# Performance work log

Measured on AMD Instinct MI355X. Metric: run time of the kernel, lower is better.

## Reference

```python
import jax, jax.numpy as jnp
import numpy as np

B, C, L = 8, 256, 2048
D = C // 8  # q/k channel dim = 32


def setup_inputs() -> dict:
    key = jax.random.key(0)
    kx, kq, kk, kv, kg = jax.random.split(key, 5)
    kq1, kq2 = jax.random.split(kq)
    kk1, kk2 = jax.random.split(kk)
    kv1, kv2 = jax.random.split(kv)
    s = 0.05
    return {
        "x": jax.random.normal(kx, (B, C, L), dtype=jnp.float32),
        "Wq": jax.random.normal(kq1, (D, C), dtype=jnp.float32) * s,
        "bq": jax.random.normal(kq2, (D,), dtype=jnp.float32) * s,
        "Wk": jax.random.normal(kk1, (D, C), dtype=jnp.float32) * s,
        "bk": jax.random.normal(kk2, (D,), dtype=jnp.float32) * s,
        "Wv": jax.random.normal(kv1, (C, C), dtype=jnp.float32) * s,
        "bv": jax.random.normal(kv2, (C,), dtype=jnp.float32) * s,
        "gamma": jax.random.normal(kg, (1,), dtype=jnp.float32) * 0.1,
    }


def reference(x, Wq, bq, Wk, bk, Wv, bv, gamma):
    # 1x1 Conv1d == per-position channel matmul
    Q = jnp.einsum("dc,bcl->bld", Wq, x) + bq            # (B, L, D)
    K = jnp.einsum("dc,bcl->bdl", Wk, x) + bk[:, None]   # (B, D, L)
    V = jnp.einsum("oc,bcl->bol", Wv, x) + bv[:, None]   # (B, C, L)
    scale = jnp.float32(1.0 / np.sqrt(D))
    # attn[b, i, j]: softmax over j (keys)
    attn = jax.nn.softmax(jnp.einsum("bid,bdj->bij", Q, K) * scale, axis=-1)
    # out = V @ attn^T : out[b, c, i] = sum_j V[b, c, j] * attn[b, i, j]
    out = jnp.einsum("bcj,bij->bci", V, attn)            # (B, C, L)
    return gamma * out + x
```

## Files before the change

### kernel.cpp

```cpp
#include <hip/hip_runtime.h>
#include <stdint.h>


#define BB 8
#define CC 256
#define LL 2048
#define DD 32

typedef unsigned short u16;
typedef __attribute__((ext_vector_type(8))) short short8;
typedef __attribute__((ext_vector_type(4))) float f32x4;

#define SCALE_LOG2E 0.2550348612f

static __device__ __forceinline__ uint32_t pack2bf16(float hi, float lo) {
    return (__float_as_uint(hi) & 0xFFFF0000u) | (__float_as_uint(lo) >> 16);
}

static __device__ __forceinline__ float fexp2(float v) {
#if __has_builtin(__builtin_amdgcn_exp2f)
    return __builtin_amdgcn_exp2f(v);
#else
    return exp2f(v);
#endif
}

static __device__ __forceinline__ float frcp(float v) {
#if __has_builtin(__builtin_amdgcn_rcpf)
    return __builtin_amdgcn_rcpf(v);
#else
    return 1.0f / v;
#endif
}

__global__ __launch_bounds__(256) void prep_w_kernel(
    const float* __restrict__ Wq, const float* __restrict__ Wk,
    const float* __restrict__ Wv, u16* __restrict__ Wh)
{
    int idx = blockIdx.x * 256 + threadIdx.x;
    int r = idx >> 6;
    int c4 = (idx & 63) << 2;
    const float* src;
    if (r < 32)       src = Wq + (size_t)r * CC + c4;
    else if (r < 64)  src = Wk + (size_t)(r - 32) * CC + c4;
    else              src = Wv + (size_t)(r - 64) * CC + c4;
    float4 v = *(const float4*)src;
    uint2 o;
    o.x = pack2bf16(v.y, v.x);
    o.y = pack2bf16(v.w, v.z);
    *(uint2*)(Wh + (size_t)r * CC + c4) = o;
}

__global__ __launch_bounds__(512, 2) void proj_kernel(
    const float* __restrict__ x, const u16* __restrict__ Wh,
    const float* __restrict__ bq, const float* __restrict__ bk,
    const float* __restrict__ bv,
    u16* __restrict__ Qh, u16* __restrict__ Kth, u16* __restrict__ Vh)
{
    __shared__ u16 xls[32 * 264];
    const int blk = blockIdx.x;
    const int b = blk & 7;
    const int l0 = (blk >> 3) << 5;
    const int tid = threadIdx.x;
    const int w = tid >> 6;
    const int lane = tid & 63;
    const int ln = lane & 15;
    const int q = lane >> 4;

#pragma unroll
    for (int cc = 0; cc < 4; ++cc) {
        const int c = cc * 64 + (tid >> 3);
        const int l4 = (tid & 7) * 4;
        const float4 v = *(const float4*)(x + ((size_t)(b * CC + c)) * LL + l0 + l4);
        xls[(l4 + 0) * 264 + c] = (u16)(__float_as_uint(v.x) >> 16);
        xls[(l4 + 1) * 264 + c] = (u16)(__float_as_uint(v.y) >> 16);
        xls[(l4 + 2) * 264 + c] = (u16)(__float_as_uint(v.z) >> 16);
        xls[(l4 + 3) * 264 + c] = (u16)(__float_as_uint(v.w) >> 16);
    }
    __syncthreads();

    const int wl = w & 1;
    const int wm = w >> 1;
    const int mbase = wm * 80;
    const int l = l0 + wl * 16 + ln;

    f32x4 acc[5];
#pragma unroll
    for (int i = 0; i < 5; ++i) acc[i] = (f32x4){0.f, 0.f, 0.f, 0.f};

#pragma unroll
    for (int c0 = 0; c0 < CC; c0 += 32) {
        const short8 bf = *(const short8*)(&xls[(wl * 16 + ln) * 264 + c0 + q * 8]);
#pragma unroll
        for (int mt = 0; mt < 5; ++mt) {
            const short8 af = *(const short8*)(Wh + (size_t)(mbase + mt * 16 + ln) * CC + c0 + q * 8);
            acc[mt] = __builtin_amdgcn_mfma_f32_16x16x32_bf16(af, bf, acc[mt], 0, 0, 0);
        }
    }

#pragma unroll
    for (int mt = 0; mt < 5; ++mt) {
        const int rg = mbase + mt * 16 + q * 4;
        if (rg < 32) {
            float v0 = (acc[mt][0] + bq[rg + 0]) * SCALE_LOG2E;
            float v1 = (acc[mt][1] + bq[rg + 1]) * SCALE_LOG2E;
            float v2 = (acc[mt][2] + bq[rg + 2]) * SCALE_LOG2E;
            float v3 = (acc[mt][3] + bq[rg + 3]) * SCALE_LOG2E;
            uint2 o; o.x = pack2bf16(v1, v0); o.y = pack2bf16(v3, v2);
            *(uint2*)(Qh + ((size_t)(b * LL) + l) * DD + rg) = o;
        } else if (rg < 64) {
            const int rk = rg - 32;
            float v0 = acc[mt][0] + bk[rk + 0];
            float v1 = acc[mt][1] + bk[rk + 1];
            float v2 = acc[mt][2] + bk[rk + 2];
            float v3 = acc[mt][3] + bk[rk + 3];
            uint2 o; o.x = pack2bf16(v1, v0); o.y = pack2bf16(v3, v2);
            *(uint2*)(Kth + ((size_t)(b * LL) + l) * DD + rk) = o;
        } else {
            const int cv = rg - 64;
#pragma unroll
            for (int rr = 0; rr < 4; ++rr) {
                const float v = acc[mt][rr] + bv[cv + rr];
                Vh[((size_t)(b * CC) + cv + rr) * LL + l] = (u16)(__float_as_uint(v) >> 16);
            }
        }
    }
}

__global__ __launch_bounds__(512, 1) void attn_kernel(
    const u16* __restrict__ Qh, const u16* __restrict__ Kth,
    const u16* __restrict__ Vh, const float* __restrict__ x,
    const float* __restrict__ gamma, float* __restrict__ out)
{
    __shared__ u16 pbuf[8 * 64 * 40];
    __shared__ float obuf[256 * 68];
    __shared__ float lbuf[8 * 64];

    const int blk = blockIdx.x;
    const int b = blk & 7;
    const int i0 = (blk >> 3) << 6;
    const int tid = threadIdx.x;
    const int w = tid >> 6;
    const int wc = w >> 2;
    const int wj = w & 3;
    const int lane = tid & 63;
    const int ln = lane & 15;
    const int q = lane >> 4;

    u16* pb = pbuf + w * (64 * 40);
    const u16* Qb = Qh + ((size_t)(b * LL) + i0) * DD;
    const u16* Kb = Kth + (size_t)(b * LL) * DD;
    const u16* Vb = Vh + ((size_t)(b * CC) + wc * 128) * LL;

    short8 qf[4];
#pragma unroll
    for (int it = 0; it < 4; ++it)
        qf[it] = *(const short8*)(Qb + (size_t)(it * 16 + ln) * DD + q * 8);

    const f32x4 zf = {0.f, 0.f, 0.f, 0.f};
    f32x4 oacc[8][4];
#pragma unroll
    for (int a = 0; a < 8; ++a)
#pragma unroll
        for (int c = 0; c < 4; ++c) oacc[a][c] = zf;
    float lsum[4] = {0.f, 0.f, 0.f, 0.f};

    int jb = wj * 32;
    short8 kf0 = *(const short8*)(Kb + (size_t)(jb + ln) * DD + q * 8);
    short8 kf1 = *(const short8*)(Kb + (size_t)(jb + 16 + ln) * DD + q * 8);

    for (int n = 0; n < 16; ++n) {
        jb = n * 128 + wj * 32;
        const int jnx = (n < 15) ? (n + 1) * 128 + wj * 32 : jb;

        short8 vf[8];
#pragma unroll
        for (int ct = 0; ct < 8; ++ct)
            vf[ct] = *(const short8*)(Vb + (size_t)(ct * 16 + ln) * LL + jb + q * 8);
        const short8 kn0 = *(const short8*)(Kb + (size_t)(jnx + ln) * DD + q * 8);
        const short8 kn1 = *(const short8*)(Kb + (size_t)(jnx + 16 + ln) * DD + q * 8);

#pragma unroll
        for (int jt = 0; jt < 2; ++jt) {
            const short8 kf = jt ? kf1 : kf0;
#pragma unroll
            for (int it = 0; it < 4; ++it) {
                const f32x4 st = __builtin_amdgcn_mfma_f32_16x16x32_bf16(kf, qf[it], zf, 0, 0, 0);
                const float e0 = fexp2(st[0]), e1 = fexp2(st[1]);
                const float e2 = fexp2(st[2]), e3 = fexp2(st[3]);
                lsum[it] += (e0 + e1) + (e2 + e3);
                uint2 d; d.x = pack2bf16(e1, e0); d.y = pack2bf16(e3, e2);
                *(uint2*)(&pb[(it * 16 + ln) * 40 + jt * 16 + q * 4]) = d;
            }
        }

        short8 pf[4];
#pragma unroll
        for (int it = 0; it < 4; ++it)
            pf[it] = *(const short8*)(&pb[(it * 16 + ln) * 40 + q * 8]);

#pragma unroll
        for (int ct = 0; ct < 8; ++ct)
#pragma unroll
            for (int it = 0; it < 4; ++it)
                oacc[ct][it] = __builtin_amdgcn_mfma_f32_16x16x32_bf16(vf[ct], pf[it], oacc[ct][it], 0, 0, 0);

        kf0 = kn0; kf1 = kn1;
    }

#pragma unroll
    for (int it = 0; it < 4; ++it) {
        float s = lsum[it];
        s += __shfl_xor(s, 16);
        s += __shfl_xor(s, 32);
        lsum[it] = s;
    }
    if (q == 0) {
#pragma unroll
        for (int it = 0; it < 4; ++it) lbuf[w * 64 + it * 16 + ln] = lsum[it];
    }

#pragma unroll
    for (int p = 0; p < 4; ++p) {
        if (wj == p) {
#pragma unroll
            for (int ct = 0; ct < 8; ++ct)
#pragma unroll
                for (int it = 0; it < 4; ++it) {
                    const int i = it * 16 + ln;
#pragma unroll
                    for (int r = 0; r < 4; ++r) {
                        const int c = wc * 128 + ct * 16 + q * 4 + r;
                        if (p == 0) obuf[c * 68 + i] = oacc[ct][it][r];
                        else        obuf[c * 68 + i] += oacc[ct][it][r];
                    }
                }
        }
        __syncthreads();
    }

    const float g = gamma[0];
    const int i4 = (tid & 15) * 4;
    float4 sv = {0.f, 0.f, 0.f, 0.f};
#pragma unroll
    for (int ww = 0; ww < 8; ++ww) {
        const float4 lv = *(const float4*)&lbuf[ww * 64 + i4];
        sv.x += lv.x; sv.y += lv.y; sv.z += lv.z; sv.w += lv.w;
    }
    float4 li;
    li.x = 2.0f * frcp(sv.x); li.y = 2.0f * frcp(sv.y);
    li.z = 2.0f * frcp(sv.z); li.w = 2.0f * frcp(sv.w);

#pragma unroll
    for (int cc = 0; cc < 8; ++cc) {
        const int c = cc * 32 + (tid >> 4);
        const float4 ov = *(const float4*)&obuf[c * 68 + i4];
        const size_t idx = ((size_t)(b * CC + c)) * LL + i0 + i4;
        const float4 xv = *(const float4*)(x + idx);
        float4 o;
        o.x = g * (ov.x * li.x) + xv.x;
        o.y = g * (ov.y * li.y) + xv.y;
        o.z = g * (ov.z * li.z) + xv.z;
        o.w = g * (ov.w * li.w) + xv.w;
        *(float4*)(out + idx) = o;
    }
}

extern "C" void kernel_launch(void* const* d_in, const int* in_sizes, int n_in,
                              void* d_out, int out_size, void* d_ws, size_t ws_size,
                              hipStream_t stream)
{
    const float* x     = (const float*)d_in[0];
    const float* Wq    = (const float*)d_in[1];
    const float* bq    = (const float*)d_in[2];
    const float* Wk    = (const float*)d_in[3];
    const float* bk    = (const float*)d_in[4];
    const float* Wv    = (const float*)d_in[5];
    const float* bv    = (const float*)d_in[6];
    const float* gamma = (const float*)d_in[7];
    float* out = (float*)d_out;

    uint8_t* ws = (uint8_t*)d_ws;
    u16* Wh  = (u16*)(ws + 0x000000);
    u16* Qh  = (u16*)(ws + 0x040000);
    u16* Kth = (u16*)(ws + 0x140000);
    u16* Vh  = (u16*)(ws + 0x240000);

    prep_w_kernel<<<80, 256, 0, stream>>>(Wq, Wk, Wv, Wh);
    proj_kernel<<<512, 512, 0, stream>>>(x, Wh, bq, bk, bv, Qh, Kth, Vh);
    attn_kernel<<<256, 512, 0, stream>>>(Qh, Kth, Vh, x, gamma, out);
}
```

Baseline: 149.4 us.

## Repartition attention across waves with shared P tile and no cross-wave reduction

The attention kernel now processes 32 queries per block over 512 blocks. Each of the 8 waves computes scores for a distinct 16-key slice and writes exp values into a double-buffered shared P tile. After a barrier, each wave multiplies its own 32 V channels against the full 128-key P tile. This removes the duplicated score/exp work across channel halves and the serialized four-phase shared-memory output reduction. In exchange it adds a block-wide barrier per key step, uses scalar output stores, and raises launch bounds to allow more resident blocks.

```diff
diff --git a/kernel.cpp b/kernel.cpp
--- a/kernel.cpp
+++ b/kernel.cpp
@@ -127,143 +127,116 @@
     }
 }
 
-__global__ __launch_bounds__(512, 1) void attn_kernel(
+#define PJ 136
+
+__global__ __launch_bounds__(512, 4) void attn_kernel(
     const u16* __restrict__ Qh, const u16* __restrict__ Kth,
     const u16* __restrict__ Vh, const float* __restrict__ x,
     const float* __restrict__ gamma, float* __restrict__ out)
 {
-    __shared__ u16 pbuf[8 * 64 * 40];
-    __shared__ float obuf[256 * 68];
-    __shared__ float lbuf[8 * 64];
+    __shared__ __attribute__((aligned(16))) u16 pbuf[2][32][PJ];
+    __shared__ float lbuf[8][32];
 
     const int blk = blockIdx.x;
     const int b = blk & 7;
-    const int i0 = (blk >> 3) << 6;
+    const int i0 = (blk >> 3) << 5;
     const int tid = threadIdx.x;
     const int w = tid >> 6;
-    const int wc = w >> 2;
-    const int wj = w & 3;
     const int lane = tid & 63;
     const int ln = lane & 15;
     const int q = lane >> 4;
 
-    u16* pb = pbuf + w * (64 * 40);
     const u16* Qb = Qh + ((size_t)(b * LL) + i0) * DD;
-    const u16* Kb = Kth + (size_t)(b * LL) * DD;
-    const u16* Vb = Vh + ((size_t)(b * CC) + wc * 128) * LL;
-
-    short8 qf[4];
-#pragma unroll
-    for (int it = 0; it < 4; ++it)
+    const u16* Kb = Kth + ((size_t)(b * LL) + w * 16 + ln) * DD + q * 8;
+    const u16* Vb = Vh + ((size_t)(b * CC) + w * 32) * LL;
+
+    short8 qf[2];
+#pragma unroll
+    for (int it = 0; it < 2; ++it)
         qf[it] = *(const short8*)(Qb + (size_t)(it * 16 + ln) * DD + q * 8);
 
     const f32x4 zf = {0.f, 0.f, 0.f, 0.f};
-    f32x4 oacc[8][4];
-#pragma unroll
-    for (int a = 0; a < 8; ++a)
-#pragma unroll
-        for (int c = 0; c < 4; ++c) oacc[a][c] = zf;
-    float lsum[4] = {0.f, 0.f, 0.f, 0.f};
-
-    int jb = wj * 32;
-    short8 kf0 = *(const short8*)(Kb + (size_t)(jb + ln) * DD + q * 8);
-    short8 kf1 = *(const short8*)(Kb + (size_t)(jb + 16 + ln) * DD + q * 8);
+    f32x4 oacc[2][2];
+#pragma unroll
+    for (int a = 0; a < 2; ++a)
+#pragma unroll
+        for (int c = 0; c < 2; ++c) oacc[a][c] = zf;
+    float lsum[2] = {0.f, 0.f};
+
+    short8 kf = *(const short8*)(Kb);
 
     for (int n = 0; n < 16; ++n) {
-        jb = n * 128 + wj * 32;
-        const int jnx = (n < 15) ? (n + 1) * 128 + wj * 32 : jb;
-
-        short8 vf[8];
-#pragma unroll
-        for (int ct = 0; ct < 8; ++ct)
-            vf[ct] = *(const short8*)(Vb + (size_t)(ct * 16 + ln) * LL + jb + q * 8);
-        const short8 kn0 = *(const short8*)(Kb + (size_t)(jnx + ln) * DD + q * 8);
-        const short8 kn1 = *(const short8*)(Kb + (size_t)(jnx + 16 + ln) * DD + q * 8);
-
-#pragma unroll
-        for (int jt = 0; jt < 2; ++jt) {
-            const short8 kf = jt ? kf1 : kf0;
-#pragma unroll
-            for (int it = 0; it < 4; ++it) {
-                const f32x4 st = __builtin_amdgcn_mfma_f32_16x16x32_bf16(kf, qf[it], zf, 0, 0, 0);
-                const float e0 = fexp2(st[0]), e1 = fexp2(st[1]);
-                const float e2 = fexp2(st[2]), e3 = fexp2(st[3]);
-                lsum[it] += (e0 + e1) + (e2 + e3);
-                uint2 d; d.x = pack2bf16(e1, e0); d.y = pack2bf16(e3, e2);
-                *(uint2*)(&pb[(it * 16 + ln) * 40 + jt * 16 + q * 4]) = d;
+        const int jb = n * 128;
+
+        short8 vf[2][4];
+#pragma unroll
+        for (int ct = 0; ct < 2; ++ct)
+#pragma unroll
+            for (int kk = 0; kk < 4; ++kk)
+                vf[ct][kk] = *(const short8*)(Vb + (size_t)(ct * 16 + ln) * LL + jb + kk * 32 + q * 8);
+        const short8 kn = *(const short8*)(Kb + (size_t)((n < 15 ? n + 1 : n) * 128) * DD);
+
+        u16* ps = &pbuf[n & 1][0][0];
+#pragma unroll
+        for (int it = 0; it < 2; ++it) {
+            const f32x4 st = __builtin_amdgcn_mfma_f32_16x16x32_bf16(kf, qf[it], zf, 0, 0, 0);
+            const float e0 = fexp2(st[0]), e1 = fexp2(st[1]);
+            const float e2 = fexp2(st[2]), e3 = fexp2(st[3]);
+            lsum[it] += (e0 + e1) + (e2 + e3);
+            uint2 d; d.x = pack2bf16(e1, e0); d.y = pack2bf16(e3, e2);
+            *(uint2*)(&ps[(it * 16 + ln) * PJ + w * 16 + q * 4]) = d;
+        }
+        __syncthreads();
+
+        __builtin_amdgcn_s_setprio(1);
+#pragma unroll
+        for (int kk = 0; kk < 4; ++kk) {
+            const short8 pf0 = *(const short8*)(&ps[(size_t)ln * PJ + kk * 32 + q * 8]);
+            const short8 pf1 = *(const short8*)(&ps[(size_t)(16 + ln) * PJ + kk * 32 + q * 8]);
+#pragma unroll
+            for (int ct = 0; ct < 2; ++ct) {
+                oacc[ct][0] = __builtin_amdgcn_mfma_f32_16x16x32_bf16(vf[ct][kk], pf0, oacc[ct][0], 0, 0, 0);
+                oacc[ct][1] = __builtin_amdgcn_mfma_f32_16x16x32_bf16(vf[ct][kk], pf1, oacc[ct][1], 0, 0, 0);
             }
         }
-
-        short8 pf[4];
-#pragma unroll
-        for (int it = 0; it < 4; ++it)
-            pf[it] = *(const short8*)(&pb[(it * 16 + ln) * 40 + q * 8]);
-
-#pragma unroll
-        for (int ct = 0; ct < 8; ++ct)
-#pragma unroll
-            for (int it = 0; it < 4; ++it)
-                oacc[ct][it] = __builtin_amdgcn_mfma_f32_16x16x32_bf16(vf[ct], pf[it], oacc[ct][it], 0, 0, 0);
-
-        kf0 = kn0; kf1 = kn1;
-    }
-
-#pragma unroll
-    for (int it = 0; it < 4; ++it) {
+        __builtin_amdgcn_s_setprio(0);
+        kf = kn;
+    }
+
+#pragma unroll
+    for (int it = 0; it < 2; ++it) {
         float s = lsum[it];
         s += __shfl_xor(s, 16);
         s += __shfl_xor(s, 32);
         lsum[it] = s;
     }
     if (q == 0) {
-#pragma unroll
-        for (int it = 0; it < 4; ++it) lbuf[w * 64 + it * 16 + ln] = lsum[it];
-    }
-
-#pragma unroll
-    for (int p = 0; p < 4; ++p) {
-        if (wj == p) {
-#pragma unroll
-            for (int ct = 0; ct < 8; ++ct)
-#pragma unroll
-                for (int it = 0; it < 4; ++it) {
-                    const int i = it * 16 + ln;
-#pragma unroll
-                    for (int r = 0; r < 4; ++r) {
-                        const int c = wc * 128 + ct * 16 + q * 4 + r;
-                        if (p == 0) obuf[c * 68 + i] = oacc[ct][it][r];
-                        else        obuf[c * 68 + i] += oacc[ct][it][r];
-                    }
-                }
-        }
-        __syncthreads();
+        lbuf[w][ln] = lsum[0];
+        lbuf[w][16 + ln] = lsum[1];
+    }
+    __syncthreads();
+
+    float linv[2];
+#pragma unroll
+    for (int it = 0; it < 2; ++it) {
+        float s = 0.f;
+#pragma unroll
+        for (int w8 = 0; w8 < 8; ++w8) s += lbuf[w8][it * 16 + ln];
+        linv[it] = frcp(s);
     }
 
     const float g = gamma[0];
-    const int i4 = (tid & 15) * 4;
-    float4 sv = {0.f, 0.f, 0.f, 0.f};
-#pragma unroll
-    for (int ww = 0; ww < 8; ++ww) {
-        const float4 lv = *(const float4*)&lbuf[ww * 64 + i4];
-        sv.x += lv.x; sv.y += lv.y; sv.z += lv.z; sv.w += lv.w;
-    }
-    float4 li;
-    li.x = 2.0f * frcp(sv.x); li.y = 2.0f * frcp(sv.y);
-    li.z = 2.0f * frcp(sv.z); li.w = 2.0f * frcp(sv.w);
-
-#pragma unroll
-    for (int cc = 0; cc < 8; ++cc) {
-        const int c = cc * 32 + (tid >> 4);
-        const float4 ov = *(const float4*)&obuf[c * 68 + i4];
-        const size_t idx = ((size_t)(b * CC + c)) * LL + i0 + i4;
-        const float4 xv = *(const float4*)(x + idx);
-        float4 o;
-        o.x = g * (ov.x * li.x) + xv.x;
-        o.y = g * (ov.y * li.y) + xv.y;
-        o.z = g * (ov.z * li.z) + xv.z;
-        o.w = g * (ov.w * li.w) + xv.w;
-        *(float4*)(out + idx) = o;
-    }
+#pragma unroll
+    for (int ct = 0; ct < 2; ++ct)
+#pragma unroll
+        for (int it = 0; it < 2; ++it) {
+#pragma unroll
+            for (int r = 0; r < 4; ++r) {
+                const int c = w * 32 + ct * 16 + q * 4 + r;
+                const size_t idx = ((size_t)(b * CC + c)) * LL + i0 + it * 16 + ln;
+                out[idx] = g * (oacc[ct][it][r] * linv[it]) + x[idx];
+            }
+        }
 }
 
 extern "C" void kernel_launch(void* const* d_in, const int* in_sizes, int n_in,
@@ -288,5 +261,5 @@
 
     prep_w_kernel<<<80, 256, 0, stream>>>(Wq, Wk, Wv, Wh);
     proj_kernel<<<512, 512, 0, stream>>>(x, Wh, bq, bk, bv, Qh, Kth, Vh);
-    attn_kernel<<<256, 512, 0, stream>>>(Qh, Kth, Vh, x, gamma, out);
-}
+    attn_kernel<<<512, 512, 0, stream>>>(Qh, Kth, Vh, x, gamma, out);
+}
```

After: 171.0 us. 1.14x slower.

## Halve attention query tile to 32 rows and raise occupancy with 512 blocks

Applied to the files above, without the earlier changes.

The attention kernel now processes 32 query rows per block instead of 64. This doubles the grid to 512 blocks and shrinks the accumulators, LDS buffers and register footprint, with launch bounds changed to allow 4 blocks per CU. The K software prefetch is dropped, and the V loads are split into two halves so the second half is issued after the score/exp phase. The intent is better latency hiding and CU fill through occupancy. In exchange, each block reuses K and V over half as many queries, doubling K/V reads across the grid.

```diff
diff --git a/kernel.cpp b/kernel.cpp
--- a/kernel.cpp
+++ b/kernel.cpp
@@ -127,18 +127,18 @@
     }
 }
 
-__global__ __launch_bounds__(512, 1) void attn_kernel(
+__global__ __launch_bounds__(512, 4) void attn_kernel(
     const u16* __restrict__ Qh, const u16* __restrict__ Kth,
     const u16* __restrict__ Vh, const float* __restrict__ x,
     const float* __restrict__ gamma, float* __restrict__ out)
 {
-    __shared__ u16 pbuf[8 * 64 * 40];
-    __shared__ float obuf[256 * 68];
-    __shared__ float lbuf[8 * 64];
+    __shared__ __attribute__((aligned(16))) u16 pbuf[8][32][40];
+    __shared__ float obuf[256][36];
+    __shared__ float lbuf[8][32];
 
     const int blk = blockIdx.x;
     const int b = blk & 7;
-    const int i0 = (blk >> 3) << 6;
+    const int i0 = (blk >> 3) << 5;
     const int tid = threadIdx.x;
     const int w = tid >> 6;
     const int wc = w >> 2;
@@ -147,44 +147,39 @@
     const int ln = lane & 15;
     const int q = lane >> 4;
 
-    u16* pb = pbuf + w * (64 * 40);
+    u16* pb = &pbuf[w][0][0];
     const u16* Qb = Qh + ((size_t)(b * LL) + i0) * DD;
     const u16* Kb = Kth + (size_t)(b * LL) * DD;
     const u16* Vb = Vh + ((size_t)(b * CC) + wc * 128) * LL;
 
-    short8 qf[4];
-#pragma unroll
-    for (int it = 0; it < 4; ++it)
+    short8 qf[2];
+#pragma unroll
+    for (int it = 0; it < 2; ++it)
         qf[it] = *(const short8*)(Qb + (size_t)(it * 16 + ln) * DD + q * 8);
 
     const f32x4 zf = {0.f, 0.f, 0.f, 0.f};
-    f32x4 oacc[8][4];
+    f32x4 oacc[8][2];
 #pragma unroll
     for (int a = 0; a < 8; ++a)
 #pragma unroll
-        for (int c = 0; c < 4; ++c) oacc[a][c] = zf;
-    float lsum[4] = {0.f, 0.f, 0.f, 0.f};
-
-    int jb = wj * 32;
-    short8 kf0 = *(const short8*)(Kb + (size_t)(jb + ln) * DD + q * 8);
-    short8 kf1 = *(const short8*)(Kb + (size_t)(jb + 16 + ln) * DD + q * 8);
+        for (int c = 0; c < 2; ++c) oacc[a][c] = zf;
+    float lsum[2] = {0.f, 0.f};
 
     for (int n = 0; n < 16; ++n) {
-        jb = n * 128 + wj * 32;
-        const int jnx = (n < 15) ? (n + 1) * 128 + wj * 32 : jb;
-
-        short8 vf[8];
-#pragma unroll
-        for (int ct = 0; ct < 8; ++ct)
-            vf[ct] = *(const short8*)(Vb + (size_t)(ct * 16 + ln) * LL + jb + q * 8);
-        const short8 kn0 = *(const short8*)(Kb + (size_t)(jnx + ln) * DD + q * 8);
-        const short8 kn1 = *(const short8*)(Kb + (size_t)(jnx + 16 + ln) * DD + q * 8);
+        const int jb = n * 128 + wj * 32;
+
+        short8 vf0[4];
+#pragma unroll
+        for (int ct = 0; ct < 4; ++ct)
+            vf0[ct] = *(const short8*)(Vb + (size_t)(ct * 16 + ln) * LL + jb + q * 8);
+        const short8 kf0 = *(const short8*)(Kb + (size_t)(jb + ln) * DD + q * 8);
+        const short8 kf1 = *(const short8*)(Kb + (size_t)(jb + 16 + ln) * DD + q * 8);
 
 #pragma unroll
         for (int jt = 0; jt < 2; ++jt) {
             const short8 kf = jt ? kf1 : kf0;
 #pragma unroll
-            for (int it = 0; it < 4; ++it) {
+            for (int it = 0; it < 2; ++it) {
                 const f32x4 st = __builtin_amdgcn_mfma_f32_16x16x32_bf16(kf, qf[it], zf, 0, 0, 0);
                 const float e0 = fexp2(st[0]), e1 = fexp2(st[1]);
                 const float e2 = fexp2(st[2]), e3 = fexp2(st[3]);
@@ -194,30 +189,38 @@
             }
         }
 
-        short8 pf[4];
-#pragma unroll
-        for (int it = 0; it < 4; ++it)
+        short8 vf1[4];
+#pragma unroll
+        for (int ct = 0; ct < 4; ++ct)
+            vf1[ct] = *(const short8*)(Vb + (size_t)((ct + 4) * 16 + ln) * LL + jb + q * 8);
+
+        short8 pf[2];
+#pragma unroll
+        for (int it = 0; it < 2; ++it)
             pf[it] = *(const short8*)(&pb[(it * 16 + ln) * 40 + q * 8]);
 
 #pragma unroll
-        for (int ct = 0; ct < 8; ++ct)
-#pragma unroll
-            for (int it = 0; it < 4; ++it)
-                oacc[ct][it] = __builtin_amdgcn_mfma_f32_16x16x32_bf16(vf[ct], pf[it], oacc[ct][it], 0, 0, 0);
-
-        kf0 = kn0; kf1 = kn1;
-    }
-
-#pragma unroll
-    for (int it = 0; it < 4; ++it) {
+        for (int ct = 0; ct < 4; ++ct)
+#pragma unroll
+            for (int it = 0; it < 2; ++it)
+                oacc[ct][it] = __builtin_amdgcn_mfma_f32_16x16x32_bf16(vf0[ct], pf[it], oacc[ct][it], 0, 0, 0);
+#pragma unroll
+        for (int ct = 0; ct < 4; ++ct)
+#pragma unroll
+            for (int it = 0; it < 2; ++it)
+                oacc[4 + ct][it] = __builtin_amdgcn_mfma_f32_16x16x32_bf16(vf1[ct], pf[it], oacc[4 + ct][it], 0, 0, 0);
+    }
+
+#pragma unroll
+    for (int it = 0; it < 2; ++it) {
         float s = lsum[it];
         s += __shfl_xor(s, 16);
         s += __shfl_xor(s, 32);
         lsum[it] = s;
     }
     if (q == 0) {
-#pragma unroll
-        for (int it = 0; it < 4; ++it) lbuf[w * 64 + it * 16 + ln] = lsum[it];
+        lbuf[w][ln] = lsum[0];
+        lbuf[w][16 + ln] = lsum[1];
     }
 
 #pragma unroll
@@ -226,13 +229,13 @@
 #pragma unroll
             for (int ct = 0; ct < 8; ++ct)
 #pragma unroll
-                for (int it = 0; it < 4; ++it) {
+                for (int it = 0; it < 2; ++it) {
                     const int i = it * 16 + ln;
 #pragma unroll
                     for (int r = 0; r < 4; ++r) {
                         const int c = wc * 128 + ct * 16 + q * 4 + r;
-                        if (p == 0) obuf[c * 68 + i] = oacc[ct][it][r];
-                        else        obuf[c * 68 + i] += oacc[ct][it][r];
+                        if (p == 0) obuf[c][i] = oacc[ct][it][r];
+                        else        obuf[c][i] += oacc[ct][it][r];
                     }
                 }
         }
@@ -240,11 +243,11 @@
     }
 
     const float g = gamma[0];
-    const int i4 = (tid & 15) * 4;
+    const int i4 = (tid & 7) * 4;
     float4 sv = {0.f, 0.f, 0.f, 0.f};
 #pragma unroll
     for (int ww = 0; ww < 8; ++ww) {
-        const float4 lv = *(const float4*)&lbuf[ww * 64 + i4];
+        const float4 lv = *(const float4*)&lbuf[ww][i4];
         sv.x += lv.x; sv.y += lv.y; sv.z += lv.z; sv.w += lv.w;
     }
     float4 li;
@@ -252,9 +255,9 @@
     li.z = 2.0f * frcp(sv.z); li.w = 2.0f * frcp(sv.w);
 
 #pragma unroll
-    for (int cc = 0; cc < 8; ++cc) {
-        const int c = cc * 32 + (tid >> 4);
-        const float4 ov = *(const float4*)&obuf[c * 68 + i4];
+    for (int cc = 0; cc < 4; ++cc) {
+        const int c = cc * 64 + (tid >> 3);
+        const float4 ov = *(const float4*)&obuf[c][i4];
         const size_t idx = ((size_t)(b * CC + c)) * LL + i0 + i4;
         const float4 xv = *(const float4*)(x + idx);
         float4 o;
@@ -288,5 +291,5 @@
 
     prep_w_kernel<<<80, 256, 0, stream>>>(Wq, Wk, Wv, Wh);
     proj_kernel<<<512, 512, 0, stream>>>(x, Wh, bq, bk, bv, Qh, Kth, Vh);
-    attn_kernel<<<256, 512, 0, stream>>>(Qh, Kth, Vh, x, gamma, out);
-}
+    attn_kernel<<<512, 512, 0, stream>>>(Qh, Kth, Vh, x, gamma, out);
+}
```

After: 174.8 us. 1.17x slower.

## Software-pipeline score and PV phases with double-buffered P; coalesce V stores

Applied to the files above, without the earlier changes.

The attention loop now computes the exp-scores for the next key block into a second LDS P buffer while the PV MFMAs for the current block run. This lets exp/VALU work interleave with matrix work, and K is prefetched two blocks ahead. The projection kernel stages V through LDS and writes it with 16-byte coalesced rows instead of scattered 2-byte stores. The cost is more LDS per block (a doubled pbuf plus a vls buffer) and some extra register pressure.

```diff
diff --git a/kernel.cpp b/kernel.cpp
--- a/kernel.cpp
+++ b/kernel.cpp
@@ -58,6 +58,7 @@
     u16* __restrict__ Qh, u16* __restrict__ Kth, u16* __restrict__ Vh)
 {
     __shared__ u16 xls[32 * 264];
+    __shared__ __attribute__((aligned(16))) u16 vls[256 * 40];
     const int blk = blockIdx.x;
     const int b = blk & 7;
     const int l0 = (blk >> 3) << 5;
@@ -83,6 +84,7 @@
     const int wm = w >> 1;
     const int mbase = wm * 80;
     const int l = l0 + wl * 16 + ln;
+    const int li = wl * 16 + ln;
 
     f32x4 acc[5];
 #pragma unroll
@@ -121,9 +123,21 @@
 #pragma unroll
             for (int rr = 0; rr < 4; ++rr) {
                 const float v = acc[mt][rr] + bv[cv + rr];
-                Vh[((size_t)(b * CC) + cv + rr) * LL + l] = (u16)(__float_as_uint(v) >> 16);
+                vls[(cv + rr) * 40 + li] = (u16)(__float_as_uint(v) >> 16);
             }
         }
+    }
+
+    __syncthreads();
+    {
+        const int row = tid >> 1;
+        const int h = (tid & 1) * 16;
+        const u16* src = &vls[row * 40 + h];
+        const uint4 v0 = *(const uint4*)(src);
+        const uint4 v1 = *(const uint4*)(src + 8);
+        uint4* dst = (uint4*)(Vh + ((size_t)(b * CC) + row) * LL + l0 + h);
+        dst[0] = v0;
+        dst[1] = v1;
     }
 }
 
@@ -132,7 +146,7 @@
     const u16* __restrict__ Vh, const float* __restrict__ x,
     const float* __restrict__ gamma, float* __restrict__ out)
 {
-    __shared__ u16 pbuf[8 * 64 * 40];
+    __shared__ __attribute__((aligned(16))) u16 pbuf[2][8][64 * 40];
     __shared__ float obuf[256 * 68];
     __shared__ float lbuf[8 * 64];
 
@@ -147,7 +161,6 @@
     const int ln = lane & 15;
     const int q = lane >> 4;
 
-    u16* pb = pbuf + w * (64 * 40);
     const u16* Qb = Qh + ((size_t)(b * LL) + i0) * DD;
     const u16* Kb = Kth + (size_t)(b * LL) * DD;
     const u16* Vb = Vh + ((size_t)(b * CC) + wc * 128) * LL;
@@ -165,24 +178,11 @@
         for (int c = 0; c < 4; ++c) oacc[a][c] = zf;
     float lsum[4] = {0.f, 0.f, 0.f, 0.f};
 
-    int jb = wj * 32;
-    short8 kf0 = *(const short8*)(Kb + (size_t)(jb + ln) * DD + q * 8);
-    short8 kf1 = *(const short8*)(Kb + (size_t)(jb + 16 + ln) * DD + q * 8);
-
-    for (int n = 0; n < 16; ++n) {
-        jb = n * 128 + wj * 32;
-        const int jnx = (n < 15) ? (n + 1) * 128 + wj * 32 : jb;
-
-        short8 vf[8];
-#pragma unroll
-        for (int ct = 0; ct < 8; ++ct)
-            vf[ct] = *(const short8*)(Vb + (size_t)(ct * 16 + ln) * LL + jb + q * 8);
-        const short8 kn0 = *(const short8*)(Kb + (size_t)(jnx + ln) * DD + q * 8);
-        const short8 kn1 = *(const short8*)(Kb + (size_t)(jnx + 16 + ln) * DD + q * 8);
-
+    auto Sphase = [&](int slot, short8 ka, short8 kb) {
+        u16* pw = &pbuf[slot][w][0];
 #pragma unroll
         for (int jt = 0; jt < 2; ++jt) {
-            const short8 kf = jt ? kf1 : kf0;
+            const short8 kf = jt ? kb : ka;
 #pragma unroll
             for (int it = 0; it < 4; ++it) {
                 const f32x4 st = __builtin_amdgcn_mfma_f32_16x16x32_bf16(kf, qf[it], zf, 0, 0, 0);
@@ -190,14 +190,37 @@
                 const float e2 = fexp2(st[2]), e3 = fexp2(st[3]);
                 lsum[it] += (e0 + e1) + (e2 + e3);
                 uint2 d; d.x = pack2bf16(e1, e0); d.y = pack2bf16(e3, e2);
-                *(uint2*)(&pb[(it * 16 + ln) * 40 + jt * 16 + q * 4]) = d;
+                *(uint2*)(&pw[(it * 16 + ln) * 40 + jt * 16 + q * 4]) = d;
             }
         }
-
+    };
+
+    {
+        const short8 k0a = *(const short8*)(Kb + (size_t)(wj * 32 + ln) * DD + q * 8);
+        const short8 k0b = *(const short8*)(Kb + (size_t)(wj * 32 + 16 + ln) * DD + q * 8);
+        Sphase(0, k0a, k0b);
+    }
+    short8 kAa = *(const short8*)(Kb + (size_t)(128 + wj * 32 + ln) * DD + q * 8);
+    short8 kAb = *(const short8*)(Kb + (size_t)(128 + wj * 32 + 16 + ln) * DD + q * 8);
+
+    for (int n = 0; n < 15; ++n) {
+        const int jb = n * 128 + wj * 32;
+        const int jb2 = ((n <= 13) ? (n + 2) : 15) * 128 + wj * 32;
+
+        short8 vf[8];
+#pragma unroll
+        for (int ct = 0; ct < 8; ++ct)
+            vf[ct] = *(const short8*)(Vb + (size_t)(ct * 16 + ln) * LL + jb + q * 8);
+        const short8 kBa = *(const short8*)(Kb + (size_t)(jb2 + ln) * DD + q * 8);
+        const short8 kBb = *(const short8*)(Kb + (size_t)(jb2 + 16 + ln) * DD + q * 8);
+
+        const u16* pr = &pbuf[n & 1][w][0];
         short8 pf[4];
 #pragma unroll
         for (int it = 0; it < 4; ++it)
-            pf[it] = *(const short8*)(&pb[(it * 16 + ln) * 40 + q * 8]);
+            pf[it] = *(const short8*)(&pr[(it * 16 + ln) * 40 + q * 8]);
+
+        Sphase((n + 1) & 1, kAa, kAb);
 
 #pragma unroll
         for (int ct = 0; ct < 8; ++ct)
@@ -205,7 +228,25 @@
             for (int it = 0; it < 4; ++it)
                 oacc[ct][it] = __builtin_amdgcn_mfma_f32_16x16x32_bf16(vf[ct], pf[it], oacc[ct][it], 0, 0, 0);
 
-        kf0 = kn0; kf1 = kn1;
+        kAa = kBa; kAb = kBb;
+    }
+
+    {
+        const int jb = 15 * 128 + wj * 32;
+        short8 vf[8];
+#pragma unroll
+        for (int ct = 0; ct < 8; ++ct)
+            vf[ct] = *(const short8*)(Vb + (size_t)(ct * 16 + ln) * LL + jb + q * 8);
+        const u16* pr = &pbuf[1][w][0];
+        short8 pf[4];
+#pragma unroll
+        for (int it = 0; it < 4; ++it)
+            pf[it] = *(const short8*)(&pr[(it * 16 + ln) * 40 + q * 8]);
+#pragma unroll
+        for (int ct = 0; ct < 8; ++ct)
+#pragma unroll
+            for (int it = 0; it < 4; ++it)
+                oacc[ct][it] = __builtin_amdgcn_mfma_f32_16x16x32_bf16(vf[ct], pf[it], oacc[ct][it], 0, 0, 0);
     }
 
 #pragma unroll
```

New measurement: 153.3 us. 1.03x slower.
